# Optimization experiments

Hardware: AMD Instinct MI355X
Metric: run time of the kernel (lower is better)

Reference implementation:

```python
import jax, jax.numpy as jnp
import numpy as np

N = 4608      # total nodes (48 graphs x 96 nodes)
B = 48
NPG = 96
D = 512       # vec_dim
XD = 16       # x_dim
E = N * 32    # GAT edges
L = 6         # GAT layers


def _w(k, shape, fan_in):
    return jax.random.normal(k, shape, jnp.float32) * (1.0 / np.sqrt(fan_in))


def setup_inputs() -> dict:
    key = jax.random.key(0)
    ks = jax.random.split(key, 24)
    x = jax.random.normal(ks[0], (N, XD), jnp.float32)
    xyz = jax.random.normal(ks[1], (N, 3), jnp.float32)
    edge_index = jax.random.randint(ks[2], (2, E), 0, N, dtype=jnp.int32)
    ptr = (jnp.arange(B + 1) * NPG).astype(jnp.int32)
    # complete graph with replacement per segment (torch.combinations order: i<=j)
    i, j = np.triu_indices(NPG)
    offs = (np.arange(B) * NPG)[:, None]
    cloud_edge_index = jnp.asarray(
        np.stack([(i[None, :] + offs).reshape(-1), (j[None, :] + offs).reshape(-1)]),
        jnp.int32)
    return {
        'x': x, 'edge_index': edge_index, 'ptr': ptr, 'xyz': xyz,
        'cloud_edge_index': cloud_edge_index,
        'x_proj_w': _w(ks[3], (XD, D), XD), 'x_proj_b': jnp.zeros((D,), jnp.float32),
        'gat_wl': _w(ks[4], (L, D, D), D), 'gat_bl': jnp.zeros((L, D), jnp.float32),
        'gat_wr': _w(ks[5], (L, D, D), D), 'gat_br': jnp.zeros((L, D), jnp.float32),
        'gat_att': _w(ks[6], (L, D), D), 'gat_bias': jnp.zeros((L, D), jnp.float32),
        'gat_ln_g': jnp.ones((L - 1, D), jnp.float32), 'gat_ln_b': jnp.zeros((L - 1, D), jnp.float32),
        'cg_xyz_w': _w(ks[7], (3, D), 3),
        'cg_bn_g': jnp.ones((D,), jnp.float32), 'cg_bn_b': jnp.zeros((D,), jnp.float32),
        'cg_lin1_w': _w(ks[8], (D, D), D), 'cg_lin1_b': jnp.zeros((D,), jnp.float32),
        'cg_ln_g': jnp.ones((D,), jnp.float32), 'cg_ln_b': jnp.zeros((D,), jnp.float32),
        'lin_w': _w(ks[9], (D, D), D), 'lin_b': jnp.zeros((D,), jnp.float32),
        'bn_g': jnp.ones((D,), jnp.float32), 'bn_b': jnp.zeros((D,), jnp.float32),
    }


def _batchnorm(t, g, b):
    mu = t.mean(0)
    v = ((t - mu) ** 2).mean(0)
    return (t - mu) / jnp.sqrt(v + 1e-5) * g + b


def _forward(x, edge_index, cloud_edge_index, x_proj_w, x_proj_b, gat_wl, gat_bl,
             gat_wr, gat_br, gat_att, gat_bias, gat_ln_g, gat_ln_b, cg_xyz_w,
             cg_bn_g, cg_bn_b, cg_lin1_w, cg_lin1_b, cg_ln_g, cg_ln_b,
             lin_w, lin_b, bn_g, bn_b, xyz):
    n = x.shape[0]
    h = x @ x_proj_w + x_proj_b  # [N, D]
    # ---- GATv2 stack (heads=1, self-loops added, eval mode: no dropout) ----
    loops = jnp.arange(n, dtype=edge_index.dtype)
    ei = jnp.concatenate([edge_index, jnp.stack([loops, loops])], axis=1)
    src, dst = ei[0], ei[1]
    xg = h
    for l in range(L):
        xl = xg @ gat_wl[l] + gat_bl[l]
        xr = xg @ gat_wr[l] + gat_br[l]
        e = jax.nn.leaky_relu(xl[src] + xr[dst], 0.2) @ gat_att[l]  # [E+N]
        m = jax.ops.segment_max(e, dst, num_segments=n)
        ew = jnp.exp(e - m[dst])
        den = jax.ops.segment_sum(ew, dst, num_segments=n)
        alpha = ew / den[dst]
        out = jax.ops.segment_sum(alpha[:, None] * xl[src], dst, num_segments=n) + gat_bias[l]
        if l < L - 1:
            # PyG LayerNorm, mode='graph', batch=None: normalize over all elements
            mu = out.mean()
            sd = jnp.sqrt(((out - mu) ** 2).mean())
            out = (out - mu) / (sd + 1e-5) * gat_ln_g[l] + gat_ln_b[l]
            out = jax.nn.relu(out)
        xg = out
    # ---- CloudGraph (complete graph gather-compute-scatter) ----
    a, b = cloud_edge_index[0], cloud_edge_index[1]
    rx = h[a] - h[b]          # [Ec, D]
    rz = xyz[a] - xyz[b]      # [Ec, 3]
    sq = (rz ** 2).sum(-1)
    dist = jnp.where(sq > 0, jnp.sqrt(jnp.where(sq > 0, sq, 1.0)), 0.0)
    w = jnp.exp(-dist)[:, None]
    p1 = jax.ops.segment_sum(jax.nn.relu((w * rx) @ cg_lin1_w + cg_lin1_b), a, num_segments=n)
    mu1 = p1.mean(-1, keepdims=True)
    v1 = ((p1 - mu1) ** 2).mean(-1, keepdims=True)
    ln1 = (p1 - mu1) / jnp.sqrt(v1 + 1e-5) * cg_ln_g + cg_ln_b
    p2 = jax.ops.segment_sum(jax.nn.relu(rz @ cg_xyz_w), a, num_segments=n)
    xc = h + ln1 + _batchnorm(p2, cg_bn_g, cg_bn_b)
    # ---- fuse + final norm ----
    return _batchnorm((h + xg + xc) @ lin_w + lin_b, bn_g, bn_b)


def reference(x, edge_index, ptr, xyz, cloud_edge_index, x_proj_w, x_proj_b,
              gat_wl, gat_bl, gat_wr, gat_br, gat_att, gat_bias, gat_ln_g,
              gat_ln_b, cg_xyz_w, cg_bn_g, cg_bn_b, cg_lin1_w, cg_lin1_b,
              cg_ln_g, cg_ln_b, lin_w, lin_b, bn_g, bn_b):
    return _forward(x, edge_index, cloud_edge_index, x_proj_w, x_proj_b, gat_wl,
                    gat_bl, gat_wr, gat_br, gat_att, gat_bias, gat_ln_g,
                    gat_ln_b, cg_xyz_w, cg_bn_g, cg_bn_b, cg_lin1_w, cg_lin1_b,
                    cg_ln_g, cg_ln_b, lin_w, lin_b, bn_g, bn_b, xyz)
```

## Files before the change

kernel.cpp:

```cpp
#include <hip/hip_runtime.h>
#include <hip/hip_bf16.h>

#define NN 4608
#define BG 48
#define NPG 96
#define DD 512
#define XDIM 16
#define EREAL 147456
#define NLAYER 6
#define NK 262144
#define TRIU 4656

typedef __hip_bfloat16 bf16;
typedef short short8 __attribute__((ext_vector_type(8)));
typedef short shortx4 __attribute__((ext_vector_type(4)));
typedef float f32x4 __attribute__((ext_vector_type(4)));
typedef float f32x2 __attribute__((ext_vector_type(2)));

__device__ __forceinline__ float s2f(short s) {
  return __uint_as_float(((unsigned int)(unsigned short)s) << 16);
}
__device__ __forceinline__ short f2bs(float f) {
  bf16 h = __float2bfloat16(f);
  short s;
  __builtin_memcpy(&s, &h, 2);
  return s;
}
__device__ __forceinline__ void f8x4(unsigned int w, float* o) {
  f32x2 a = __builtin_amdgcn_cvt_pk_f32_fp8(w, false);
  f32x2 b = __builtin_amdgcn_cvt_pk_f32_fp8(w, true);
  o[0] = a[0]; o[1] = a[1]; o[2] = b[0]; o[3] = b[1];
}

typedef const __attribute__((address_space(1))) unsigned int ga_u32;
typedef __attribute__((address_space(3))) unsigned int ls_u32;
__device__ __forceinline__ void gl16(const void* g, void* l) {
  __builtin_amdgcn_global_load_lds((ga_u32*)g, (ls_u32*)l, 16, 0, 0);
}

__global__ __launch_bounds__(256) void k_wt(const float* __restrict__ wl,
                                            const float* __restrict__ wr,
                                            const float* __restrict__ cg,
                                            const float* __restrict__ lin,
                                            bf16* __restrict__ Wt,
                                            int* __restrict__ counts,
                                            float* __restrict__ statsAll) {
  if (blockIdx.z == 0) {
    int id = (blockIdx.y * 16 + blockIdx.x) * 256 + threadIdx.x;
    if (id < NN) counts[id] = 0;
    if (id < 5 * 32) statsAll[id] = 0.f;
  }
  __shared__ float tile[32][33];
  int z = blockIdx.z;
  const float* src = (z < 6) ? wl + (size_t)z * NK
                   : (z < 12) ? wr + (size_t)(z - 6) * NK
                   : (z == 12) ? cg : lin;
  bf16* dst = Wt + (size_t)z * NK;
  int c = threadIdx.x & 31;
  int r0 = threadIdx.x >> 5;
  int bx = blockIdx.x * 32, by = blockIdx.y * 32;
#pragma unroll
  for (int i = 0; i < 4; i++) {
    int r = r0 + i * 8;
    tile[r][c] = src[(size_t)(by + r) * 512 + bx + c];
  }
  __syncthreads();
#pragma unroll
  for (int i = 0; i < 4; i++) {
    int r = r0 + i * 8;
    dst[(size_t)(bx + r) * 512 + by + c] = __float2bfloat16(tile[c][r]);
  }
}

__global__ void k_xproj(const float* __restrict__ x, const float* __restrict__ w,
                        const float* __restrict__ b, const int* __restrict__ ei,
                        const float* __restrict__ xyz,
                        bf16* __restrict__ h_bf, int* __restrict__ counts,
                        float* __restrict__ ep) {
  int i = blockIdx.x * blockDim.x + threadIdx.x;
  if (i >= NN * DD) return;
  if (i < EREAL) atomicAdd(&counts[ei[EREAL + i]], 1);
  if (i < NN * NPG) {
    int n = i / NPG, e = i - n * NPG;
    int p = n % NPG;
    if (e < NPG - p) {
      int g = n / NPG;
      int slot = g * TRIU + p * NPG - (p * (p - 1)) / 2 + e;
      int j = n + e;
      float dx = xyz[n * 3] - xyz[j * 3];
      float dy = xyz[n * 3 + 1] - xyz[j * 3 + 1];
      float dz = xyz[n * 3 + 2] - xyz[j * 3 + 2];
      float sq = dx * dx + dy * dy + dz * dz;
      float dist = (sq > 0.f) ? sqrtf(sq) : 0.f;
      float4 v;
      v.x = dx; v.y = dy; v.z = dz; v.w = __expf(-dist);
      *(float4*)&ep[(size_t)slot * 4] = v;
    }
  }
  int n = i >> 9, d = i & 511;
  float acc = b[d];
#pragma unroll
  for (int k = 0; k < XDIM; k++) acc += x[n * XDIM + k] * w[k * DD + d];
  h_bf[i] = __float2bfloat16(acc);
}

__global__ void k_scan(const int* __restrict__ counts, int* offsets, int* cursor) {
  __shared__ int part[256];
  int t = threadIdx.x;
  int base = t * 18;
  int s = 0;
#pragma unroll
  for (int i = 0; i < 18; i++) s += counts[base + i];
  part[t] = s;
  __syncthreads();
  for (int off = 1; off < 256; off <<= 1) {
    int v = part[t];
    int u = (t >= off) ? part[t - off] : 0;
    __syncthreads();
    part[t] = v + u;
    __syncthreads();
  }
  int run = t ? part[t - 1] : 0;
#pragma unroll
  for (int i = 0; i < 18; i++) {
    offsets[base + i] = run;
    cursor[base + i] = run;
    run += counts[base + i];
  }
  if (t == 0) offsets[NN] = EREAL;
}

__global__ __launch_bounds__(256) void k_ln(bf16* __restrict__ xg,
                                            const float* __restrict__ stats,
                                            const float* __restrict__ g,
                                            const float* __restrict__ b,
                                            const float* __restrict__ p2a,
                                            const float* __restrict__ p2b,
                                            float* __restrict__ colsum,
                                            float* __restrict__ colsq) {
  if ((int)blockIdx.x >= 1152) {
    int r0 = (blockIdx.x - 1152) * 32;
    int c0 = threadIdx.x;
    float s0 = 0.f, q0 = 0.f, s1 = 0.f, q1 = 0.f;
    for (int r = r0; r < r0 + 32; ++r) {
      float v = p2a[(size_t)r * 512 + c0] + p2b[(size_t)r * 512 + c0];
      s0 += v; q0 += v * v;
      float w = p2a[(size_t)r * 512 + c0 + 256] + p2b[(size_t)r * 512 + c0 + 256];
      s1 += w; q1 += w * w;
    }
    atomicAdd(&colsum[c0], s0);
    atomicAdd(&colsq[c0], q0);
    atomicAdd(&colsum[c0 + 256], s1);
    atomicAdd(&colsq[c0 + 256], q1);
    return;
  }
  float s = 0.f, ss = 0.f;
#pragma unroll
  for (int i = 0; i < 16; i++) { s += stats[i]; ss += stats[16 + i]; }
  const float invM = 1.f / ((float)NN * (float)DD);
  float mu = s * invM;
  float var = ss * invM - mu * mu;
  float sd = sqrtf(fmaxf(var, 0.f));
  float inv = 1.f / (sd + 1e-5f);
  int i = blockIdx.x * 256 + threadIdx.x;
  int base = i * 8;
  int d0 = base & 511;
  short8 raw = *(const short8*)&xg[base];
  short8 pk;
#pragma unroll
  for (int k = 0; k < 8; k++) {
    float t = fmaxf((s2f(raw[k]) - mu) * inv * g[d0 + k] + b[d0 + k], 0.f);
    pk[k] = f2bs(t);
  }
  *(short8*)&xg[base] = pk;
}

__device__ __forceinline__ void gemm_tile(
    const bf16* __restrict__ Abf, const bf16* __restrict__ B,
    const float* __restrict__ bias,
    float* __restrict__ C, bf16* __restrict__ Cb, unsigned char* __restrict__ Cf8,
    float* __restrict__ csum, float* __restrict__ csq,
    int m0, int n0, bf16* As, bf16* Bs, float* cs, float* cq) {
  int tid = threadIdx.x;
  int lane = tid & 63, wid = tid >> 6;
  int mh = (wid >> 1) * 64, nh = (wid & 1) * 32;
  int l15 = lane & 15, quad = lane >> 4;
  int lr8 = lane >> 3, ls8 = lane & 7;
  int c16l = ls8 ^ lr8;
  int swzr = (l15 & 7) * 8;

  if (csum && tid < 64) { cs[tid] = 0.f; cq[tid] = 0.f; }

  const bf16* aSrc = Abf + (size_t)(m0 + wid * 32 + lr8) * 512 + c16l * 8;
  const bf16* bSrc = B   + (size_t)(n0 + wid * 16 + lr8) * 512 + c16l * 8;

#define STAGE(bi, kt) do {                                                   \
    gl16(aSrc + (kt) * 64,            As + (bi) * 8192 + (wid * 32     ) * 64); \
    gl16(aSrc + (kt) * 64 +  8 * 512, As + (bi) * 8192 + (wid * 32 +  8) * 64); \
    gl16(aSrc + (kt) * 64 + 16 * 512, As + (bi) * 8192 + (wid * 32 + 16) * 64); \
    gl16(aSrc + (kt) * 64 + 24 * 512, As + (bi) * 8192 + (wid * 32 + 24) * 64); \
    gl16(bSrc + (kt) * 64,            Bs + (bi) * 4096 + (wid * 16     ) * 64); \
    gl16(bSrc + (kt) * 64 +  8 * 512, Bs + (bi) * 4096 + (wid * 16 +  8) * 64); \
  } while (0)

  f32x4 acc[4][2];
#pragma unroll
  for (int mt = 0; mt < 4; mt++)
#pragma unroll
    for (int nt = 0; nt < 2; nt++) acc[mt][nt] = (f32x4)0.f;

  STAGE(0, 0);
  __syncthreads();

#pragma unroll
  for (int kt = 0; kt < 8; kt++) {
    const int cur = kt & 1;
    if (kt < 7) STAGE(cur ^ 1, kt + 1);
    short8 af[2][4], bfr[2][2];
#pragma unroll
    for (int kk = 0; kk < 2; kk++) {
#pragma unroll
      for (int mt = 0; mt < 4; mt++)
        af[kk][mt] = *(const short8*)&As[cur * 8192 + (mh + mt * 16 + l15) * 64 +
                                        (((kk * 4 + quad) * 8) ^ swzr)];
#pragma unroll
      for (int nt = 0; nt < 2; nt++)
        bfr[kk][nt] = *(const short8*)&Bs[cur * 4096 + (nh + nt * 16 + l15) * 64 +
                                         (((kk * 4 + quad) * 8) ^ swzr)];
    }
#pragma unroll
    for (int kk = 0; kk < 2; kk++)
#pragma unroll
      for (int mt = 0; mt < 4; mt++)
#pragma unroll
        for (int nt = 0; nt < 2; nt++)
          acc[mt][nt] = __builtin_amdgcn_mfma_f32_16x16x32_bf16(
              bfr[kk][nt], af[kk][mt], acc[mt][nt], 0, 0, 0);
    __syncthreads();
  }
#undef STAGE

  float colS[2][4] = {{0.f,0.f,0.f,0.f},{0.f,0.f,0.f,0.f}};
  float colQ[2][4] = {{0.f,0.f,0.f,0.f},{0.f,0.f,0.f,0.f}};
  float bv[2][4] = {{0.f,0.f,0.f,0.f},{0.f,0.f,0.f,0.f}};
#pragma unroll
  for (int nt = 0; nt < 2; nt++) {
    if (bias) {
      float4 b4 = *(const float4*)&bias[n0 + nh + nt * 16 + quad * 4];
      bv[nt][0] = b4.x; bv[nt][1] = b4.y; bv[nt][2] = b4.z; bv[nt][3] = b4.w;
    }
  }
#pragma unroll
  for (int mt = 0; mt < 4; mt++) {
    int row = m0 + mh + mt * 16 + l15;
#pragma unroll
    for (int nt = 0; nt < 2; nt++) {
      int col0 = n0 + nh + nt * 16 + quad * 4;
      float v[4];
#pragma unroll
      for (int r2 = 0; r2 < 4; r2++) {
        v[r2] = acc[mt][nt][r2] + bv[nt][r2];
        if (csum) { colS[nt][r2] += v[r2]; colQ[nt][r2] += v[r2] * v[r2]; }
      }
      if (C) {
        float4 o; o.x = v[0]; o.y = v[1]; o.z = v[2]; o.w = v[3];
        *(float4*)&C[(size_t)row * 512 + col0] = o;
      }
      if (Cb) {
        shortx4 o;
#pragma unroll
        for (int r2 = 0; r2 < 4; r2++) o[r2] = f2bs(v[r2]);
        *(shortx4*)&Cb[(size_t)row * 512 + col0] = o;
      }
      if (Cf8) {
        unsigned int u = __builtin_amdgcn_cvt_pk_fp8_f32(v[0], v[1], 0, false);
        u = __builtin_amdgcn_cvt_pk_fp8_f32(v[2], v[3], u, true);
        *(unsigned int*)&Cf8[(size_t)row * 512 + col0] = u;
      }
    }
  }
  if (csum) {
#pragma unroll
    for (int nt = 0; nt < 2; nt++)
#pragma unroll
      for (int r2 = 0; r2 < 4; r2++) {
        atomicAdd(&cs[nh + nt * 16 + quad * 4 + r2], colS[nt][r2]);
        atomicAdd(&cq[nh + nt * 16 + quad * 4 + r2], colQ[nt][r2]);
      }
    __syncthreads();
    if (tid < 64) {
      atomicAdd(&csum[n0 + tid], cs[tid]);
      atomicAdd(&csq[n0 + tid], cq[tid]);
    }
  }
}

__global__ __launch_bounds__(256) void k_gemm(
    const bf16* __restrict__ Abf,
    const bf16* __restrict__ B0, const bf16* __restrict__ B1,
    const float* __restrict__ bias0, const float* __restrict__ bias1,
    float* __restrict__ C0,
    bf16* __restrict__ Cb0, bf16* __restrict__ Cb1,
    unsigned char* __restrict__ Cf8_0,
    float* __restrict__ csum, float* __restrict__ csq, int nzl) {
  __shared__ __align__(16) bf16 As[2 * 128 * 64];
  __shared__ __align__(16) bf16 Bs[2 * 64 * 64];
  __shared__ float cs[64], cq[64];
  int cpx = gridDim.x >> 3;
  int wgid = (blockIdx.x & 7) * cpx + (blockIdx.x >> 3);
  int mi = wgid >> nzl;
  int r = wgid & ((1 << nzl) - 1);
  int z = r >> 3;
  int m0 = mi * 128, n0 = (r & 7) * 64;
  gemm_tile(Abf, z ? B1 : B0, z ? bias1 : bias0,
            z ? nullptr : C0, z ? Cb1 : Cb0, z ? nullptr : Cf8_0,
            csum, csq, m0, n0, As, Bs, cs, cq);
}

__global__ __launch_bounds__(256) void k_gemm_l0(
    const bf16* __restrict__ h_bf,
    const bf16* __restrict__ Bl, const bf16* __restrict__ Br,
    const float* __restrict__ biasl, const float* __restrict__ biasr,
    bf16* __restrict__ xr_bf, unsigned char* __restrict__ xl_f8,
    const bf16* __restrict__ Bg1, float* __restrict__ g1f,
    float* __restrict__ zptr,
    const int* __restrict__ ei, int* __restrict__ cursor, int* __restrict__ ssrc) {
  __shared__ __align__(16) bf16 As[2 * 128 * 64];
  __shared__ __align__(16) bf16 Bs[2 * 64 * 64];
  int b = blockIdx.x;
  if (b < 576) {
    int cpx = 576 >> 3;
    int wgid = (b & 7) * cpx + (b >> 3);
    int mi = wgid >> 4;
    int r = wgid & 15;
    int z = r >> 3;
    int m0 = mi * 128, n0 = (r & 7) * 64;
    gemm_tile(h_bf, z ? Br : Bl, z ? biasr : biasl,
              nullptr, z ? xr_bf : nullptr, z ? nullptr : xl_f8,
              nullptr, nullptr, m0, n0, As, Bs, nullptr, nullptr);
  } else if (b < 864) {
    int b2 = b - 576;
    if (b2 == 0) {
      for (int i = threadIdx.x; i < 1024; i += 256) zptr[i] = 0.f;
    }
    int cpx = 288 >> 3;
    int wgid = (b2 & 7) * cpx + (b2 >> 3);
    int mi = wgid >> 3;
    int r = wgid & 7;
    int m0 = mi * 128, n0 = r * 64;
    gemm_tile(h_bf, Bg1, nullptr, g1f, nullptr, nullptr,
              nullptr, nullptr, m0, n0, As, Bs, nullptr, nullptr);
  } else {
    int e = (b - 864) * 256 + threadIdx.x;
    int s = ei[e], d = ei[EREAL + e];
    int pos = atomicAdd(&cursor[d], 1);
    ssrc[pos] = s;
  }
}

__device__ __forceinline__ void edge_block(
    const unsigned char* __restrict__ xl8, const bf16* __restrict__ xr,
    const float* __restrict__ att, const float* __restrict__ bias,
    const int* __restrict__ offs, const int* __restrict__ ssrc,
    bf16* __restrict__ out, float* __restrict__ statsOut,
    float* redS, float* redSS,
    const float* __restrict__ p1a, const float* __restrict__ p1b,
    const float* __restrict__ p2a, const float* __restrict__ p2b,
    const bf16* __restrict__ h_bf,
    const float* __restrict__ colsum, const float* __restrict__ colsq,
    const float* __restrict__ lng, const float* __restrict__ lnb,
    const float* __restrict__ bng, const float* __restrict__ bnb,
    bf16* __restrict__ s_bf, float* __restrict__ zptr) {
  if (zptr && blockIdx.x == 0) {
    for (int i = threadIdx.x; i < 1024; i += 256) zptr[i] = 0.f;
  }
  int wave = (blockIdx.x * blockDim.x + threadIdx.x) >> 6;
  int lane = threadIdx.x & 63;
  int wid = threadIdx.x >> 6;
  if (wave < NN) {
    int n = wave;
    int base = lane * 8;
    float xrv[8], attv[8], acc[8];
    short8 xr8 = *(const short8*)&xr[(size_t)n * 512 + base];
#pragma unroll
    for (int k = 0; k < 8; k++) {
      xrv[k] = s2f(xr8[k]);
      attv[k] = att[base + k];
    }
    float m0, lsum;
    {
      uint2 q = *(const uint2*)&xl8[(size_t)n * 512 + base];
      float xs[8];
      f8x4(q.x, xs);
      f8x4(q.y, xs + 4);
      float sc0 = 0.f;
#pragma unroll
      for (int k = 0; k < 8; k++) {
        acc[k] = xs[k];
        float t = xs[k] + xrv[k];
        t = (t > 0.f) ? t : 0.2f * t;
        sc0 += attv[k] * t;
      }
#pragma unroll
      for (int off = 32; off >= 1; off >>= 1) sc0 += __shfl_xor(sc0, off, 64);
      m0 = sc0;
      lsum = 1.f;
    }
    int e0 = offs[n], e1 = offs[n + 1];
    int e = e0;
    for (; e + 3 < e1; e += 4) {
      int s0 = ssrc[e], s1 = ssrc[e + 1], s2 = ssrc[e + 2], s3 = ssrc[e + 3];
      uint2 q0 = *(const uint2*)&xl8[(size_t)s0 * 512 + base];
      uint2 q1 = *(const uint2*)&xl8[(size_t)s1 * 512 + base];
      uint2 q2 = *(const uint2*)&xl8[(size_t)s2 * 512 + base];
      uint2 q3 = *(const uint2*)&xl8[(size_t)s3 * 512 + base];
      float x0[8], x1[8], x2[8], x3[8];
      f8x4(q0.x, x0); f8x4(q0.y, x0 + 4);
      f8x4(q1.x, x1); f8x4(q1.y, x1 + 4);
      f8x4(q2.x, x2); f8x4(q2.y, x2 + 4);
      f8x4(q3.x, x3); f8x4(q3.y, x3 + 4);
      float c0 = 0.f, c1 = 0.f, c2 = 0.f, c3 = 0.f;
#pragma unroll
      for (int k = 0; k < 8; k++) {
        float t0 = x0[k] + xrv[k]; t0 = (t0 > 0.f) ? t0 : 0.2f * t0; c0 += attv[k] * t0;
        float t1 = x1[k] + xrv[k]; t1 = (t1 > 0.f) ? t1 : 0.2f * t1; c1 += attv[k] * t1;
        float t2 = x2[k] + xrv[k]; t2 = (t2 > 0.f) ? t2 : 0.2f * t2; c2 += attv[k] * t2;
        float t3 = x3[k] + xrv[k]; t3 = (t3 > 0.f) ? t3 : 0.2f * t3; c3 += attv[k] * t3;
      }
#pragma unroll
      for (int off = 32; off >= 1; off >>= 1) {
        c0 += __shfl_xor(c0, off, 64);
        c1 += __shfl_xor(c1, off, 64);
        c2 += __shfl_xor(c2, off, 64);
        c3 += __shfl_xor(c3, off, 64);
      }
      float p0 = __expf(c0 - m0), pp1 = __expf(c1 - m0);
      float pp2 = __expf(c2 - m0), p3 = __expf(c3 - m0);
      lsum += p0 + pp1 + pp2 + p3;
#pragma unroll
      for (int k = 0; k < 8; k++)
        acc[k] += p0 * x0[k] + pp1 * x1[k] + pp2 * x2[k] + p3 * x3[k];
    }
    for (; e < e1; ++e) {
      int s0 = ssrc[e];
      uint2 q = *(const uint2*)&xl8[(size_t)s0 * 512 + base];
      float x0[8];
      f8x4(q.x, x0);
      f8x4(q.y, x0 + 4);
      float sc0 = 0.f;
#pragma unroll
      for (int k = 0; k < 8; k++) {
        float t0 = x0[k] + xrv[k];
        t0 = (t0 > 0.f) ? t0 : 0.2f * t0;
        sc0 += attv[k] * t0;
      }
#pragma unroll
      for (int off = 32; off >= 1; off >>= 1) sc0 += __shfl_xor(sc0, off, 64);
      float p0 = __expf(sc0 - m0);
      lsum += p0;
#pragma unroll
      for (int k = 0; k < 8; k++) acc[k] += p0 * x0[k];
    }
    float inv = 1.f / lsum;
    float o[8];
    float s = 0.f, ss = 0.f;
    short8 o8;
#pragma unroll
    for (int k = 0; k < 8; k++) {
      o[k] = acc[k] * inv + bias[base + k];
      s += o[k];
      ss += o[k] * o[k];
      o8[k] = f2bs(o[k]);
    }
    *(short8*)&out[(size_t)n * 512 + base] = o8;
    if (statsOut) {
#pragma unroll
      for (int off = 32; off >= 1; off >>= 1) {
        s += __shfl_xor(s, off, 64);
        ss += __shfl_xor(ss, off, 64);
      }
      if (lane == 0) { redS[wid] = s; redSS[wid] = ss; }
    }
    if (s_bf) {
      size_t rb = (size_t)n * 512 + base;
      float v[8];
      float sp = 0.f;
#pragma unroll
      for (int k = 0; k < 8; k++) {
        v[k] = p1a[rb + k] + p1b[rb + k];
        sp += v[k];
      }
#pragma unroll
      for (int off = 32; off >= 1; off >>= 1) sp += __shfl_xor(sp, off, 64);
      float mu = sp * (1.f / 512.f);
      float ssp = 0.f;
#pragma unroll
      for (int k = 0; k < 8; k++) {
        float t = v[k] - mu;
        ssp += t * t;
      }
#pragma unroll
      for (int off = 32; off >= 1; off >>= 1) ssp += __shfl_xor(ssp, off, 64);
      float linv = 1.f / sqrtf(ssp * (1.f / 512.f) + 1e-5f);
      short8 hb = *(const short8*)&h_bf[rb];
      short8 e8;
#pragma unroll
      for (int k = 0; k < 8; k++) {
        int d = base + k;
        float ln1 = (v[k] - mu) * linv * lng[d] + lnb[d];
        float cmu = colsum[d] * (1.f / NN);
        float cvar = colsq[d] * (1.f / NN) - cmu * cmu;
        float cinv = 1.f / sqrtf(fmaxf(cvar, 0.f) + 1e-5f);
        float p2v = p2a[rb + k] + p2b[rb + k];
        float bnv = (p2v - cmu) * cinv * bng[d] + bnb[d];
        float outv = 2.f * s2f(hb[k]) + s2f(o8[k]) + ln1 + bnv;
        e8[k] = f2bs(outv);
      }
      *(short8*)&s_bf[rb] = e8;
    }
  }
  if (statsOut) {
    __syncthreads();
    if (threadIdx.x == 0) {
      float a = redS[0] + redS[1] + redS[2] + redS[3];
      float b = redSS[0] + redSS[1] + redSS[2] + redSS[3];
      int slot = blockIdx.x & 15;
      atomicAdd(&statsOut[slot], a);
      atomicAdd(&statsOut[16 + slot], b);
    }
  }
}

__device__ __forceinline__ void cloud_wave(
    const float* __restrict__ g1f, const float* __restrict__ ep,
    const float* __restrict__ lin1b, const float* __restrict__ w3,
    float* __restrict__ p1c, float* __restrict__ p2c, int w, int lane) {
  int qh = w & 1;
  int c = (w >> 1) & 1;
  int pi = w >> 2;
  int g = pi / 48, pp = pi % 48;
  int d0 = qh * 256 + lane * 4;
  float4 bb4 = *(const float4*)&lin1b[d0];
  float4 w04 = *(const float4*)&w3[d0];
  float4 w14 = *(const float4*)&w3[512 + d0];
  float4 w24 = *(const float4*)&w3[1024 + d0];
  float bb[4] = {bb4.x, bb4.y, bb4.z, bb4.w};
  float w0[4] = {w04.x, w04.y, w04.z, w04.w};
  float w1[4] = {w14.x, w14.y, w14.z, w14.w};
  float w2[4] = {w24.x, w24.y, w24.z, w24.w};

#pragma unroll
  for (int half = 0; half < 2; half++) {
    int p = half ? (NPG - 1 - pp) : pp;
    int n = g * NPG + p;
    int cnt = NPG - p;
    int h = cnt >> 1;
    int eBeg = c ? h : 0;
    int eEnd = c ? cnt : h;
    int slot0 = g * TRIU + p * NPG - (p * (p - 1)) / 2;
    const float* grow = &g1f[(size_t)n * 512 + d0];
    float4 g4 = *(const float4*)grow;
    float gi[4] = {g4.x, g4.y, g4.z, g4.w};
    float a1[4] = {0.f,0.f,0.f,0.f}, a2[4] = {0.f,0.f,0.f,0.f};
    float b1[4] = {0.f,0.f,0.f,0.f}, b2[4] = {0.f,0.f,0.f,0.f};
    int e = eBeg;
    for (; e + 3 < eEnd; e += 4) {
      int sb = __builtin_amdgcn_readfirstlane(slot0 + e);
      float4 pa = *(const float4*)&ep[(size_t)sb * 4];
      float4 pb = *(const float4*)&ep[(size_t)(sb + 1) * 4];
      float4 pc = *(const float4*)&ep[(size_t)(sb + 2) * 4];
      float4 pd = *(const float4*)&ep[(size_t)(sb + 3) * 4];
      float4 xa = *(const float4*)&grow[(size_t)e * 512];
      float4 xb = *(const float4*)&grow[(size_t)(e + 1) * 512];
      float4 xc = *(const float4*)&grow[(size_t)(e + 2) * 512];
      float4 xd = *(const float4*)&grow[(size_t)(e + 3) * 512];
      float xaf[4] = {xa.x, xa.y, xa.z, xa.w};
      float xbf[4] = {xb.x, xb.y, xb.z, xb.w};
      float xcf[4] = {xc.x, xc.y, xc.z, xc.w};
      float xdf[4] = {xd.x, xd.y, xd.z, xd.w};
      float t;
#pragma unroll
      for (int k = 0; k < 4; k++) {
        t = fmaf(pa.w, gi[k] - xaf[k], bb[k]); a1[k] += fmaxf(t, 0.f);
        t = fmaf(pb.w, gi[k] - xbf[k], bb[k]); b1[k] += fmaxf(t, 0.f);
        t = fmaf(pc.w, gi[k] - xcf[k], bb[k]); a1[k] += fmaxf(t, 0.f);
        t = fmaf(pd.w, gi[k] - xdf[k], bb[k]); b1[k] += fmaxf(t, 0.f);
        t = pa.x * w0[k] + pa.y * w1[k] + pa.z * w2[k]; a2[k] += fmaxf(t, 0.f);
        t = pb.x * w0[k] + pb.y * w1[k] + pb.z * w2[k]; b2[k] += fmaxf(t, 0.f);
        t = pc.x * w0[k] + pc.y * w1[k] + pc.z * w2[k]; a2[k] += fmaxf(t, 0.f);
        t = pd.x * w0[k] + pd.y * w1[k] + pd.z * w2[k]; b2[k] += fmaxf(t, 0.f);
      }
    }
    for (; e < eEnd; ++e) {
      float4 pa = *(const float4*)&ep[(size_t)(slot0 + e) * 4];
      float4 xa = *(const float4*)&grow[(size_t)e * 512];
      float xaf[4] = {xa.x, xa.y, xa.z, xa.w};
      float t;
#pragma unroll
      for (int k = 0; k < 4; k++) {
        t = fmaf(pa.w, gi[k] - xaf[k], bb[k]); a1[k] += fmaxf(t, 0.f);
        t = pa.x * w0[k] + pa.y * w1[k] + pa.z * w2[k]; a2[k] += fmaxf(t, 0.f);
      }
    }
    float4 o1, o2;
    o1.x = a1[0] + b1[0]; o1.y = a1[1] + b1[1];
    o1.z = a1[2] + b1[2]; o1.w = a1[3] + b1[3];
    o2.x = a2[0] + b2[0]; o2.y = a2[1] + b2[1];
    o2.z = a2[2] + b2[2]; o2.w = a2[3] + b2[3];
    *(float4*)&p1c[(size_t)n * 512 + d0] = o1;
    *(float4*)&p2c[(size_t)n * 512 + d0] = o2;
  }
}

__global__ __launch_bounds__(256) void k_gat_edge(
    const unsigned char* __restrict__ xl8, const bf16* __restrict__ xr,
    const float* __restrict__ att, const float* __restrict__ bias,
    const int* __restrict__ offs, const int* __restrict__ ssrc,
    bf16* __restrict__ out, float* __restrict__ statsOut,
    const float* __restrict__ p1a, const float* __restrict__ p1b,
    const float* __restrict__ p2a, const float* __restrict__ p2b,
    const bf16* __restrict__ h_bf,
    const float* __restrict__ colsum, const float* __restrict__ colsq,
    const float* __restrict__ lng, const float* __restrict__ lnb,
    const float* __restrict__ bng, const float* __restrict__ bnb,
    bf16* __restrict__ s_bf, float* __restrict__ zptr,
    const float* __restrict__ g1f, const float* __restrict__ ep,
    const float* __restrict__ lin1b_c, const float* __restrict__ w3,
    float* __restrict__ cp1a, float* __restrict__ cp1b,
    float* __restrict__ cp2a, float* __restrict__ cp2b, int chunkStart) {
  __shared__ float redS[4], redSS[4];
  if ((int)blockIdx.x < 1152) {
    edge_block(xl8, xr, att, bias, offs, ssrc, out, statsOut, redS, redSS,
               p1a, p1b, p2a, p2b, h_bf, colsum, colsq, lng, lnb, bng, bnb,
               s_bf, zptr);
  } else {
    int w = ((int)blockIdx.x - 1152 + chunkStart) * 4 + (threadIdx.x >> 6);
    int c = (w >> 1) & 1;
    cloud_wave(g1f, ep, lin1b_c, w3, c ? cp1b : cp1a, c ? cp2b : cp2a,
               w, threadIdx.x & 63);
  }
}

__global__ void k_bn_out(const float* __restrict__ y, const float* __restrict__ colsum,
                         const float* __restrict__ colsq, const float* __restrict__ g,
                         const float* __restrict__ b, float* __restrict__ out) {
  int i = blockIdx.x * blockDim.x + threadIdx.x;
  if (i >= NN * DD) return;
  int d = i & 511;
  float mu = colsum[d] * (1.f / NN);
  float var = colsq[d] * (1.f / NN) - mu * mu;
  float inv = 1.f / sqrtf(fmaxf(var, 0.f) + 1e-5f);
  out[i] = (y[i] - mu) * inv * g[d] + b[d];
}

extern "C" void kernel_launch(void* const* d_in, const int* in_sizes, int n_in,
                              void* d_out, int out_size, void* d_ws, size_t ws_size,
                              hipStream_t stream) {
  const float* x = (const float*)d_in[0];
  const int* ei = (const int*)d_in[1];
  const float* xyz = (const float*)d_in[3];
  const float* x_proj_w = (const float*)d_in[5];
  const float* x_proj_b = (const float*)d_in[6];
  const float* gat_wl = (const float*)d_in[7];
  const float* gat_bl = (const float*)d_in[8];
  const float* gat_wr = (const float*)d_in[9];
  const float* gat_br = (const float*)d_in[10];
  const float* gat_att = (const float*)d_in[11];
  const float* gat_bias = (const float*)d_in[12];
  const float* gat_ln_g = (const float*)d_in[13];
  const float* gat_ln_b = (const float*)d_in[14];
  const float* cg_xyz_w = (const float*)d_in[15];
  const float* cg_bn_g = (const float*)d_in[16];
  const float* cg_bn_b = (const float*)d_in[17];
  const float* cg_lin1_w = (const float*)d_in[18];
  const float* cg_lin1_b = (const float*)d_in[19];
  const float* cg_ln_g = (const float*)d_in[20];
  const float* cg_ln_b = (const float*)d_in[21];
  const float* lin_w = (const float*)d_in[22];
  const float* lin_b = (const float*)d_in[23];
  const float* bn_g = (const float*)d_in[24];
  const float* bn_b = (const float*)d_in[25];

  const size_t ND = (size_t)NN * DD;
  char* w = (char*)d_ws;
  float* p1a = (float*)w;      w += ND * 4;
  float* p2a = (float*)w;      w += ND * 4;
  float* p1b = (float*)w;      w += ND * 4;
  float* p2b = (float*)w;      w += ND * 4;
  float* g1f = (float*)w;      w += ND * 4;
  bf16* h_bf = (bf16*)w;       w += ND * 2;
  bf16* xg_bf = (bf16*)w;      w += ND * 2;
  bf16* xr_bf = (bf16*)w;      w += ND * 2;
  unsigned char* xl_f8 = (unsigned char*)w; w += ND;
  bf16* Wt = (bf16*)w;         w += (size_t)14 * NK * 2;
  float* eparam = (float*)w;   w += (size_t)BG * TRIU * 16;
  int* counts = (int*)w;       w += NN * 4;
  int* offs = (int*)w;         w += (NN + 4) * 4;
  int* cursor = (int*)w;       w += NN * 4;
  int* ssrc = (int*)w;         w += EREAL * 4;
  float* statsAll = (float*)w; w += 5 * 32 * 4;
  float* colsum = (float*)w;   w += 512 * 4;
  float* colsq = (float*)w;    w += 512 * 4;
  float* colsum2 = (float*)w;  w += 512 * 4;
  float* colsq2 = (float*)w;   w += 512 * 4;
  float* y = p1a;
  bf16* s_bf = h_bf;

  const int TPB = 256;
  const int ND_BLK = (int)((ND + TPB - 1) / TPB);

  k_wt<<<dim3(16, 16, 14), TPB, 0, stream>>>(gat_wl, gat_wr, cg_lin1_w, lin_w, Wt,
                                             counts, statsAll);
  k_xproj<<<ND_BLK, TPB, 0, stream>>>(x, x_proj_w, x_proj_b, ei, xyz, h_bf,
                                      counts, eparam);
  k_scan<<<1, 256, 0, stream>>>(counts, offs, cursor);

  k_gemm_l0<<<1440, TPB, 0, stream>>>(h_bf, Wt, Wt + (size_t)6 * NK,
                                      gat_bl, gat_br, xr_bf, xl_f8,
                                      Wt + (size_t)12 * NK, g1f, colsum,
                                      ei, cursor, ssrc);

  for (int l = 0; l < NLAYER; l++) {
    if (l > 0) {
      k_ln<<<(l == 5) ? 1296 : 1152, TPB, 0, stream>>>(
          xg_bf, statsAll + 32 * (l - 1),
          gat_ln_g + (size_t)(l - 1) * DD, gat_ln_b + (size_t)(l - 1) * DD,
          p2a, p2b, colsum, colsq);
      k_gemm<<<576, TPB, 0, stream>>>(
          xg_bf, Wt + (size_t)l * NK, Wt + (size_t)(6 + l) * NK,
          gat_bl + l * DD, gat_br + l * DD, nullptr, nullptr, xr_bf,
          xl_f8, nullptr, nullptr, 4);
    }
    float* sOut = (l < NLAYER - 1) ? statsAll + 32 * l : nullptr;
    bool last = (l == NLAYER - 1);
    bool hasCloud = (l < 4);
    k_gat_edge<<<1152 + (hasCloud ? 576 : 0), TPB, 0, stream>>>(
        xl_f8, xr_bf, gat_att + l * DD, gat_bias + l * DD, offs, ssrc,
        xg_bf, sOut,
        last ? p1a : nullptr, last ? p1b : nullptr,
        last ? p2a : nullptr, last ? p2b : nullptr,
        last ? h_bf : nullptr,
        last ? colsum : nullptr, last ? colsq : nullptr,
        last ? cg_ln_g : nullptr, last ? cg_ln_b : nullptr,
        last ? cg_bn_g : nullptr, last ? cg_bn_b : nullptr,
        last ? s_bf : nullptr, last ? colsum2 : nullptr,
        hasCloud ? g1f : nullptr, eparam, cg_lin1_b, cg_xyz_w,
        p1a, p1b, p2a, p2b, l * 576);
  }

  k_gemm<<<288, TPB, 0, stream>>>(
      s_bf, Wt + (size_t)13 * NK, Wt + (size_t)13 * NK, lin_b, lin_b,
      y, nullptr, nullptr, nullptr, colsum2, colsq2, 3);
  k_bn_out<<<ND_BLK, TPB, 0, stream>>>(y, colsum2, colsq2, bn_g, bn_b,
                                       (float*)d_out);
}
```

Before: 496.8 us.

## Fuse GAT layer-norm+ReLU into the A-tile load of the following GEMM

Removes the standalone k_ln kernel. The next GEMM now loads raw bf16 xg rows into registers, applies the graph-level norm, affine and ReLU, and writes the result into shared memory. The p2 column-stat blocks now ride as extra blocks in the same launch. This saves a full read-modify-write pass over xg and one launch per layer. The cost is that the A operand no longer uses async global-to-LDS copies, and each N-tile block recomputes the normalisation redundantly, which adds VALU work and register pressure in the GEMM main loop.

```diff
diff --git a/kernel.cpp b/kernel.cpp
--- a/kernel.cpp
+++ b/kernel.cpp
@@ -130,16 +130,187 @@
   if (t == 0) offsets[NN] = EREAL;
 }
 
-__global__ __launch_bounds__(256) void k_ln(bf16* __restrict__ xg,
-                                            const float* __restrict__ stats,
-                                            const float* __restrict__ g,
-                                            const float* __restrict__ b,
-                                            const float* __restrict__ p2a,
-                                            const float* __restrict__ p2b,
-                                            float* __restrict__ colsum,
-                                            float* __restrict__ colsq) {
-  if ((int)blockIdx.x >= 1152) {
-    int r0 = (blockIdx.x - 1152) * 32;
+__device__ __forceinline__ void gemm_tile(
+    const bf16* __restrict__ Abf, const bf16* __restrict__ B,
+    const float* __restrict__ bias,
+    float* __restrict__ C, bf16* __restrict__ Cb, unsigned char* __restrict__ Cf8,
+    float* __restrict__ csum, float* __restrict__ csq,
+    int m0, int n0, bf16* As, bf16* Bs, float* cs, float* cq,
+    const float* __restrict__ lnG, const float* __restrict__ lnB,
+    float lnMu, float lnInv) {
+  int tid = threadIdx.x;
+  int lane = tid & 63, wid = tid >> 6;
+  int mh = (wid >> 1) * 64, nh = (wid & 1) * 32;
+  int l15 = lane & 15, quad = lane >> 4;
+  int lr8 = lane >> 3, ls8 = lane & 7;
+  int c16l = ls8 ^ lr8;
+  int swzr = (l15 & 7) * 8;
+
+  if (csum && tid < 64) { cs[tid] = 0.f; cq[tid] = 0.f; }
+
+  const bf16* aSrc = Abf + (size_t)(m0 + wid * 32 + lr8) * 512 + c16l * 8;
+  const bf16* bSrc = B   + (size_t)(n0 + wid * 16 + lr8) * 512 + c16l * 8;
+
+#define STAGE_B(bi, kt) do {                                                 \
+    gl16(bSrc + (kt) * 64,            Bs + (bi) * 4096 + (wid * 16     ) * 64); \
+    gl16(bSrc + (kt) * 64 +  8 * 512, Bs + (bi) * 4096 + (wid * 16 +  8) * 64); \
+  } while (0)
+#define STAGE_A_GL(bi, kt) do {                                              \
+    gl16(aSrc + (kt) * 64,            As + (bi) * 8192 + (wid * 32     ) * 64); \
+    gl16(aSrc + (kt) * 64 +  8 * 512, As + (bi) * 8192 + (wid * 32 +  8) * 64); \
+    gl16(aSrc + (kt) * 64 + 16 * 512, As + (bi) * 8192 + (wid * 32 + 16) * 64); \
+    gl16(aSrc + (kt) * 64 + 24 * 512, As + (bi) * 8192 + (wid * 32 + 24) * 64); \
+  } while (0)
+#define LOADA(kt, ar) do {                                                   \
+    _Pragma("unroll")                                                        \
+    for (int i2 = 0; i2 < 4; i2++)                                           \
+      ar[i2] = *(const short8*)(aSrc + (kt) * 64 + (size_t)i2 * 8 * 512);    \
+  } while (0)
+#define LNSTORE(bi, kt, ar) do {                                             \
+    int d0 = (kt) * 64 + c16l * 8;                                           \
+    float4 g1v = *(const float4*)&lnG[d0];                                   \
+    float4 g2v = *(const float4*)&lnG[d0 + 4];                               \
+    float4 b1v = *(const float4*)&lnB[d0];                                   \
+    float4 b2v = *(const float4*)&lnB[d0 + 4];                               \
+    float gg[8] = {g1v.x, g1v.y, g1v.z, g1v.w, g2v.x, g2v.y, g2v.z, g2v.w}; \
+    float bb[8] = {b1v.x, b1v.y, b1v.z, b1v.w, b2v.x, b2v.y, b2v.z, b2v.w}; \
+    _Pragma("unroll")                                                        \
+    for (int i2 = 0; i2 < 4; i2++) {                                         \
+      short8 pk;                                                             \
+      _Pragma("unroll")                                                      \
+      for (int j2 = 0; j2 < 8; j2++) {                                       \
+        float t = fmaxf((s2f(ar[i2][j2]) - lnMu) * lnInv * gg[j2] + bb[j2],  \
+                        0.f);                                                \
+        pk[j2] = f2bs(t);                                                    \
+      }                                                                      \
+      *(short8*)&As[(bi) * 8192 + (wid * 32 + i2 * 8 + lr8) * 64 + ls8 * 8] = pk; \
+    }                                                                        \
+  } while (0)
+
+  f32x4 acc[4][2];
+#pragma unroll
+  for (int mt = 0; mt < 4; mt++)
+#pragma unroll
+    for (int nt = 0; nt < 2; nt++) acc[mt][nt] = (f32x4)0.f;
+
+  short8 arP[4];
+  STAGE_B(0, 0);
+  if (lnG) {
+    LOADA(0, arP);
+    LNSTORE(0, 0, arP);
+  } else {
+    STAGE_A_GL(0, 0);
+  }
+  __syncthreads();
+
+#pragma unroll
+  for (int kt = 0; kt < 8; kt++) {
+    const int cur = kt & 1;
+    if (kt < 7) {
+      STAGE_B(cur ^ 1, kt + 1);
+      if (lnG) LOADA(kt + 1, arP);
+      else STAGE_A_GL(cur ^ 1, kt + 1);
+    }
+    short8 af[2][4], bfr[2][2];
+#pragma unroll
+    for (int kk = 0; kk < 2; kk++) {
+#pragma unroll
+      for (int mt = 0; mt < 4; mt++)
+        af[kk][mt] = *(const short8*)&As[cur * 8192 + (mh + mt * 16 + l15) * 64 +
+                                        (((kk * 4 + quad) * 8) ^ swzr)];
+#pragma unroll
+      for (int nt = 0; nt < 2; nt++)
+        bfr[kk][nt] = *(const short8*)&Bs[cur * 4096 + (nh + nt * 16 + l15) * 64 +
+                                         (((kk * 4 + quad) * 8) ^ swzr)];
+    }
+#pragma unroll
+    for (int kk = 0; kk < 2; kk++)
+#pragma unroll
+      for (int mt = 0; mt < 4; mt++)
+#pragma unroll
+        for (int nt = 0; nt < 2; nt++)
+          acc[mt][nt] = __builtin_amdgcn_mfma_f32_16x16x32_bf16(
+              bfr[kk][nt], af[kk][mt], acc[mt][nt], 0, 0, 0);
+    if (kt < 7 && lnG) LNSTORE(cur ^ 1, kt + 1, arP);
+    __syncthreads();
+  }
+#undef STAGE_B
+#undef STAGE_A_GL
+#undef LOADA
+#undef LNSTORE
+
+  float colS[2][4] = {{0.f,0.f,0.f,0.f},{0.f,0.f,0.f,0.f}};
+  float colQ[2][4] = {{0.f,0.f,0.f,0.f},{0.f,0.f,0.f,0.f}};
+  float bv[2][4] = {{0.f,0.f,0.f,0.f},{0.f,0.f,0.f,0.f}};
+#pragma unroll
+  for (int nt = 0; nt < 2; nt++) {
+    if (bias) {
+      float4 b4 = *(const float4*)&bias[n0 + nh + nt * 16 + quad * 4];
+      bv[nt][0] = b4.x; bv[nt][1] = b4.y; bv[nt][2] = b4.z; bv[nt][3] = b4.w;
+    }
+  }
+#pragma unroll
+  for (int mt = 0; mt < 4; mt++) {
+    int row = m0 + mh + mt * 16 + l15;
+#pragma unroll
+    for (int nt = 0; nt < 2; nt++) {
+      int col0 = n0 + nh + nt * 16 + quad * 4;
+      float v[4];
+#pragma unroll
+      for (int r2 = 0; r2 < 4; r2++) {
+        v[r2] = acc[mt][nt][r2] + bv[nt][r2];
+        if (csum) { colS[nt][r2] += v[r2]; colQ[nt][r2] += v[r2] * v[r2]; }
+      }
+      if (C) {
+        float4 o; o.x = v[0]; o.y = v[1]; o.z = v[2]; o.w = v[3];
+        *(float4*)&C[(size_t)row * 512 + col0] = o;
+      }
+      if (Cb) {
+        shortx4 o;
+#pragma unroll
+        for (int r2 = 0; r2 < 4; r2++) o[r2] = f2bs(v[r2]);
+        *(shortx4*)&Cb[(size_t)row * 512 + col0] = o;
+      }
+      if (Cf8) {
+        unsigned int u = __builtin_amdgcn_cvt_pk_fp8_f32(v[0], v[1], 0, false);
+        u = __builtin_amdgcn_cvt_pk_fp8_f32(v[2], v[3], u, true);
+        *(unsigned int*)&Cf8[(size_t)row * 512 + col0] = u;
+      }
+    }
+  }
+  if (csum) {
+#pragma unroll
+    for (int nt = 0; nt < 2; nt++)
+#pragma unroll
+      for (int r2 = 0; r2 < 4; r2++) {
+        atomicAdd(&cs[nh + nt * 16 + quad * 4 + r2], colS[nt][r2]);
+        atomicAdd(&cq[nh + nt * 16 + quad * 4 + r2], colQ[nt][r2]);
+      }
+    __syncthreads();
+    if (tid < 64) {
+      atomicAdd(&csum[n0 + tid], cs[tid]);
+      atomicAdd(&csq[n0 + tid], cq[tid]);
+    }
+  }
+}
+
+__global__ __launch_bounds__(256) void k_gemm(
+    const bf16* __restrict__ Abf,
+    const bf16* __restrict__ B0, const bf16* __restrict__ B1,
+    const float* __restrict__ bias0, const float* __restrict__ bias1,
+    float* __restrict__ C0,
+    bf16* __restrict__ Cb0, bf16* __restrict__ Cb1,
+    unsigned char* __restrict__ Cf8_0,
+    float* __restrict__ csum, float* __restrict__ csq, int nzl, int mainB,
+    const float* __restrict__ stats,
+    const float* __restrict__ lnG, const float* __restrict__ lnB,
+    const float* __restrict__ p2a, const float* __restrict__ p2b,
+    float* __restrict__ bnsum, float* __restrict__ bnsq) {
+  __shared__ __align__(16) bf16 As[2 * 128 * 64];
+  __shared__ __align__(16) bf16 Bs[2 * 64 * 64];
+  __shared__ float cs[64], cq[64];
+  if ((int)blockIdx.x >= mainB) {
+    int r0 = (blockIdx.x - mainB) * 32;
     int c0 = threadIdx.x;
     float s0 = 0.f, q0 = 0.f, s1 = 0.f, q1 = 0.f;
     for (int r = r0; r < r0 + 32; ++r) {
@@ -148,165 +319,24 @@
       float w = p2a[(size_t)r * 512 + c0 + 256] + p2b[(size_t)r * 512 + c0 + 256];
       s1 += w; q1 += w * w;
     }
-    atomicAdd(&colsum[c0], s0);
-    atomicAdd(&colsq[c0], q0);
-    atomicAdd(&colsum[c0 + 256], s1);
-    atomicAdd(&colsq[c0 + 256], q1);
+    atomicAdd(&bnsum[c0], s0);
+    atomicAdd(&bnsq[c0], q0);
+    atomicAdd(&bnsum[c0 + 256], s1);
+    atomicAdd(&bnsq[c0 + 256], q1);
     return;
   }
-  float s = 0.f, ss = 0.f;
-#pragma unroll
-  for (int i = 0; i < 16; i++) { s += stats[i]; ss += stats[16 + i]; }
-  const float invM = 1.f / ((float)NN * (float)DD);
-  float mu = s * invM;
-  float var = ss * invM - mu * mu;
-  float sd = sqrtf(fmaxf(var, 0.f));
-  float inv = 1.f / (sd + 1e-5f);
-  int i = blockIdx.x * 256 + threadIdx.x;
-  int base = i * 8;
-  int d0 = base & 511;
-  short8 raw = *(const short8*)&xg[base];
-  short8 pk;
-#pragma unroll
-  for (int k = 0; k < 8; k++) {
-    float t = fmaxf((s2f(raw[k]) - mu) * inv * g[d0 + k] + b[d0 + k], 0.f);
-    pk[k] = f2bs(t);
-  }
-  *(short8*)&xg[base] = pk;
-}
-
-__device__ __forceinline__ void gemm_tile(
-    const bf16* __restrict__ Abf, const bf16* __restrict__ B,
-    const float* __restrict__ bias,
-    float* __restrict__ C, bf16* __restrict__ Cb, unsigned char* __restrict__ Cf8,
-    float* __restrict__ csum, float* __restrict__ csq,
-    int m0, int n0, bf16* As, bf16* Bs, float* cs, float* cq) {
-  int tid = threadIdx.x;
-  int lane = tid & 63, wid = tid >> 6;
-  int mh = (wid >> 1) * 64, nh = (wid & 1) * 32;
-  int l15 = lane & 15, quad = lane >> 4;
-  int lr8 = lane >> 3, ls8 = lane & 7;
-  int c16l = ls8 ^ lr8;
-  int swzr = (l15 & 7) * 8;
-
-  if (csum && tid < 64) { cs[tid] = 0.f; cq[tid] = 0.f; }
-
-  const bf16* aSrc = Abf + (size_t)(m0 + wid * 32 + lr8) * 512 + c16l * 8;
-  const bf16* bSrc = B   + (size_t)(n0 + wid * 16 + lr8) * 512 + c16l * 8;
-
-#define STAGE(bi, kt) do {                                                   \
-    gl16(aSrc + (kt) * 64,            As + (bi) * 8192 + (wid * 32     ) * 64); \
-    gl16(aSrc + (kt) * 64 +  8 * 512, As + (bi) * 8192 + (wid * 32 +  8) * 64); \
-    gl16(aSrc + (kt) * 64 + 16 * 512, As + (bi) * 8192 + (wid * 32 + 16) * 64); \
-    gl16(aSrc + (kt) * 64 + 24 * 512, As + (bi) * 8192 + (wid * 32 + 24) * 64); \
-    gl16(bSrc + (kt) * 64,            Bs + (bi) * 4096 + (wid * 16     ) * 64); \
-    gl16(bSrc + (kt) * 64 +  8 * 512, Bs + (bi) * 4096 + (wid * 16 +  8) * 64); \
-  } while (0)
-
-  f32x4 acc[4][2];
-#pragma unroll
-  for (int mt = 0; mt < 4; mt++)
-#pragma unroll
-    for (int nt = 0; nt < 2; nt++) acc[mt][nt] = (f32x4)0.f;
-
-  STAGE(0, 0);
-  __syncthreads();
-
-#pragma unroll
-  for (int kt = 0; kt < 8; kt++) {
-    const int cur = kt & 1;
-    if (kt < 7) STAGE(cur ^ 1, kt + 1);
-    short8 af[2][4], bfr[2][2];
-#pragma unroll
-    for (int kk = 0; kk < 2; kk++) {
-#pragma unroll
-      for (int mt = 0; mt < 4; mt++)
-        af[kk][mt] = *(const short8*)&As[cur * 8192 + (mh + mt * 16 + l15) * 64 +
-                                        (((kk * 4 + quad) * 8) ^ swzr)];
-#pragma unroll
-      for (int nt = 0; nt < 2; nt++)
-        bfr[kk][nt] = *(const short8*)&Bs[cur * 4096 + (nh + nt * 16 + l15) * 64 +
-                                         (((kk * 4 + quad) * 8) ^ swzr)];
-    }
-#pragma unroll
-    for (int kk = 0; kk < 2; kk++)
-#pragma unroll
-      for (int mt = 0; mt < 4; mt++)
-#pragma unroll
-        for (int nt = 0; nt < 2; nt++)
-          acc[mt][nt] = __builtin_amdgcn_mfma_f32_16x16x32_bf16(
-              bfr[kk][nt], af[kk][mt], acc[mt][nt], 0, 0, 0);
-    __syncthreads();
-  }
-#undef STAGE
-
-  float colS[2][4] = {{0.f,0.f,0.f,0.f},{0.f,0.f,0.f,0.f}};
-  float colQ[2][4] = {{0.f,0.f,0.f,0.f},{0.f,0.f,0.f,0.f}};
-  float bv[2][4] = {{0.f,0.f,0.f,0.f},{0.f,0.f,0.f,0.f}};
-#pragma unroll
-  for (int nt = 0; nt < 2; nt++) {
-    if (bias) {
-      float4 b4 = *(const float4*)&bias[n0 + nh + nt * 16 + quad * 4];
-      bv[nt][0] = b4.x; bv[nt][1] = b4.y; bv[nt][2] = b4.z; bv[nt][3] = b4.w;
-    }
-  }
-#pragma unroll
-  for (int mt = 0; mt < 4; mt++) {
-    int row = m0 + mh + mt * 16 + l15;
-#pragma unroll
-    for (int nt = 0; nt < 2; nt++) {
-      int col0 = n0 + nh + nt * 16 + quad * 4;
-      float v[4];
-#pragma unroll
-      for (int r2 = 0; r2 < 4; r2++) {
-        v[r2] = acc[mt][nt][r2] + bv[nt][r2];
-        if (csum) { colS[nt][r2] += v[r2]; colQ[nt][r2] += v[r2] * v[r2]; }
-      }
-      if (C) {
-        float4 o; o.x = v[0]; o.y = v[1]; o.z = v[2]; o.w = v[3];
-        *(float4*)&C[(size_t)row * 512 + col0] = o;
-      }
-      if (Cb) {
-        shortx4 o;
-#pragma unroll
-        for (int r2 = 0; r2 < 4; r2++) o[r2] = f2bs(v[r2]);
-        *(shortx4*)&Cb[(size_t)row * 512 + col0] = o;
-      }
-      if (Cf8) {
-        unsigned int u = __builtin_amdgcn_cvt_pk_fp8_f32(v[0], v[1], 0, false);
-        u = __builtin_amdgcn_cvt_pk_fp8_f32(v[2], v[3], u, true);
-        *(unsigned int*)&Cf8[(size_t)row * 512 + col0] = u;
-      }
-    }
-  }
-  if (csum) {
-#pragma unroll
-    for (int nt = 0; nt < 2; nt++)
-#pragma unroll
-      for (int r2 = 0; r2 < 4; r2++) {
-        atomicAdd(&cs[nh + nt * 16 + quad * 4 + r2], colS[nt][r2]);
-        atomicAdd(&cq[nh + nt * 16 + quad * 4 + r2], colQ[nt][r2]);
-      }
-    __syncthreads();
-    if (tid < 64) {
-      atomicAdd(&csum[n0 + tid], cs[tid]);
-      atomicAdd(&csq[n0 + tid], cq[tid]);
-    }
-  }
-}
-
-__global__ __launch_bounds__(256) void k_gemm(
-    const bf16* __restrict__ Abf,
-    const bf16* __restrict__ B0, const bf16* __restrict__ B1,
-    const float* __restrict__ bias0, const float* __restrict__ bias1,
-    float* __restrict__ C0,
-    bf16* __restrict__ Cb0, bf16* __restrict__ Cb1,
-    unsigned char* __restrict__ Cf8_0,
-    float* __restrict__ csum, float* __restrict__ csq, int nzl) {
-  __shared__ __align__(16) bf16 As[2 * 128 * 64];
-  __shared__ __align__(16) bf16 Bs[2 * 64 * 64];
-  __shared__ float cs[64], cq[64];
-  int cpx = gridDim.x >> 3;
+  float lnMu = 0.f, lnInv = 1.f;
+  if (stats) {
+    float s = 0.f, ss = 0.f;
+#pragma unroll
+    for (int i = 0; i < 16; i++) { s += stats[i]; ss += stats[16 + i]; }
+    const float invM = 1.f / ((float)NN * (float)DD);
+    lnMu = s * invM;
+    float var = ss * invM - lnMu * lnMu;
+    float sd = sqrtf(fmaxf(var, 0.f));
+    lnInv = 1.f / (sd + 1e-5f);
+  }
+  int cpx = mainB >> 3;
   int wgid = (blockIdx.x & 7) * cpx + (blockIdx.x >> 3);
   int mi = wgid >> nzl;
   int r = wgid & ((1 << nzl) - 1);
@@ -314,7 +344,8 @@
   int m0 = mi * 128, n0 = (r & 7) * 64;
   gemm_tile(Abf, z ? B1 : B0, z ? bias1 : bias0,
             z ? nullptr : C0, z ? Cb1 : Cb0, z ? nullptr : Cf8_0,
-            csum, csq, m0, n0, As, Bs, cs, cq);
+            csum, csq, m0, n0, As, Bs, cs, cq,
+            stats ? lnG : nullptr, lnB, lnMu, lnInv);
 }
 
 __global__ __launch_bounds__(256) void k_gemm_l0(
@@ -337,7 +368,8 @@
     int m0 = mi * 128, n0 = (r & 7) * 64;
     gemm_tile(h_bf, z ? Br : Bl, z ? biasr : biasl,
               nullptr, z ? xr_bf : nullptr, z ? nullptr : xl_f8,
-              nullptr, nullptr, m0, n0, As, Bs, nullptr, nullptr);
+              nullptr, nullptr, m0, n0, As, Bs, nullptr, nullptr,
+              nullptr, nullptr, 0.f, 1.f);
   } else if (b < 864) {
     int b2 = b - 576;
     if (b2 == 0) {
@@ -349,7 +381,8 @@
     int r = wgid & 7;
     int m0 = mi * 128, n0 = r * 64;
     gemm_tile(h_bf, Bg1, nullptr, g1f, nullptr, nullptr,
-              nullptr, nullptr, m0, n0, As, Bs, nullptr, nullptr);
+              nullptr, nullptr, m0, n0, As, Bs, nullptr, nullptr,
+              nullptr, nullptr, 0.f, 1.f);
   } else {
     int e = (b - 864) * 256 + threadIdx.x;
     int s = ei[e], d = ei[EREAL + e];
@@ -722,14 +755,13 @@
 
   for (int l = 0; l < NLAYER; l++) {
     if (l > 0) {
-      k_ln<<<(l == 5) ? 1296 : 1152, TPB, 0, stream>>>(
-          xg_bf, statsAll + 32 * (l - 1),
+      k_gemm<<<576 + ((l == 5) ? 144 : 0), TPB, 0, stream>>>(
+          xg_bf, Wt + (size_t)l * NK, Wt + (size_t)(6 + l) * NK,
+          gat_bl + l * DD, gat_br + l * DD, nullptr, nullptr, xr_bf,
+          xl_f8, nullptr, nullptr, 4, 576,
+          statsAll + 32 * (l - 1),
           gat_ln_g + (size_t)(l - 1) * DD, gat_ln_b + (size_t)(l - 1) * DD,
           p2a, p2b, colsum, colsq);
-      k_gemm<<<576, TPB, 0, stream>>>(
-          xg_bf, Wt + (size_t)l * NK, Wt + (size_t)(6 + l) * NK,
-          gat_bl + l * DD, gat_br + l * DD, nullptr, nullptr, xr_bf,
-          xl_f8, nullptr, nullptr, 4);
     }
     float* sOut = (l < NLAYER - 1) ? statsAll + 32 * l : nullptr;
     bool last = (l == NLAYER - 1);
@@ -750,7 +782,8 @@
 
   k_gemm<<<288, TPB, 0, stream>>>(
       s_bf, Wt + (size_t)13 * NK, Wt + (size_t)13 * NK, lin_b, lin_b,
-      y, nullptr, nullptr, nullptr, colsum2, colsq2, 3);
+      y, nullptr, nullptr, nullptr, colsum2, colsq2, 3, 288,
+      nullptr, nullptr, nullptr, nullptr, nullptr, nullptr, nullptr);
   k_bn_out<<<ND_BLK, TPB, 0, stream>>>(y, colsum2, colsq2, bn_g, bn_b,
                                        (float*)d_out);
 }
```

New measurement: 508.8 us. +2.4%, slower.
